# Performance work log

Measured on AMD Instinct MI355X. Metric: run time of the kernel, lower is better.

The kernel has to match this reference:

```python
import jax, jax.numpy as jnp
import numpy as np

# dims: S spaces, B batch, T tokens, D = dense_dim = concept_dim, K codebook size
S, B, T, D, K = 8, 8, 2048, 64, 512
BN_EPS = 1e-3  # keras BatchNormalization default


def setup_inputs() -> dict:
    key = jax.random.key(0)
    k0, k1, k2 = jax.random.split(key, 3)
    x = jax.random.normal(k0, (B, T, D), jnp.float32)
    W = jax.random.normal(k1, (S, D, D), jnp.float32) * 0.1   # per-space Dense kernels
    b = jnp.zeros((S, D), jnp.float32)                         # per-space Dense biases
    gamma = jnp.ones((S, D), jnp.float32)                      # BN scale
    beta = jnp.zeros((S, D), jnp.float32)                      # BN shift
    bn_mean = jnp.zeros((S, D), jnp.float32)                   # BN moving mean
    bn_var = jnp.ones((S, D), jnp.float32)                     # BN moving var
    E = jax.random.normal(k2, (S, K, D), jnp.float32)          # per-space codebooks
    return dict(x=x, W=W, b=b, gamma=gamma, beta=beta,
                bn_mean=bn_mean, bn_var=bn_var, E=E)


def reference(x, W, b, gamma, beta, bn_mean, bn_var, E):
    # per-space projection: Dense -> BatchNorm (inference) -> softmax gate
    proj = jnp.einsum('btd,sde->sbte', x, W) + b[:, None, None, :]          # [S,B,T,D]
    inv = jax.lax.rsqrt(bn_var + BN_EPS)
    bn = gamma[:, None, None, :] * (proj - bn_mean[:, None, None, :]) * inv[:, None, None, :] \
         + beta[:, None, None, :]
    att = jax.nn.softmax(bn, axis=-1)
    z = x[None] * att                                                       # z_e_att, [S,B,T,D]

    # squared euclidean distance to each code; argmin(norm) == argmin(dist^2)
    d2 = (jnp.sum(z * z, axis=-1, keepdims=True)
          - 2.0 * jnp.einsum('sbtc,skc->sbtk', z, E)
          + jnp.sum(E * E, axis=-1)[:, None, None, :])                      # [S,B,T,K]
    z_k = jnp.argmin(d2, axis=-1)                                           # [S,B,T] int

    # gather nearest codes per space, then add_n over spaces (set_att != 0)
    z_q_s = E[jnp.arange(S)[:, None, None], z_k]                            # [S,B,T,D]
    z_q = jnp.sum(z_q_s, axis=0)                                            # [B,T,D]
    z_e = jnp.sum(z, axis=0)                                                # [B,T,D]
    z_k = z_k.astype(jnp.int64) if z_k.dtype != jnp.int64 else z_k          # tf.argmin -> int64
    return z_q, z_e, z_k
```

## Files before the change

kernel.cpp:

```cpp
#include <hip/hip_runtime.h>
#include <cfloat>
#include <cmath>

#define SN 8
#define DN 64
#define KN 512
#define NN 16384
#define CK 64
#define REPAIR_THR 2e-3f
#define GAP_IK 4u
#define MAXFLAG 32768

#define WS_CNT 0
#define WS_SCL 16
#define WS_OFF (16 + SN*DN)
#define WS_E2  (WS_OFF + SN*DN)
#define WS_ENT (WS_E2 + SN*KN)
#define WS_WTH (WS_ENT + MAXFLAG)
#define WS_WTL (WS_WTH + SN*64*32)
#define WS_EH  (WS_WTL + SN*64*32)
#define WS_EL  (WS_EH + SN*KN*32)
#define WS_ZP  (WS_EL + SN*KN*32)
#define WS_E2S (WS_ZP + SN*NN*DN)
#define WS_END (WS_E2S + SN*KN)

#define LDS_ZH 0
#define LDS_ZL 16384
#define LDS_TOTAL 32768

#define FB_LDS_R2    17408
#define FB_LDS_TAIL  33792
#define FB_LDS_TOTAL 34816

typedef __attribute__((ext_vector_type(8))) short bf16x8;
typedef __attribute__((ext_vector_type(4))) short s16x4;
typedef __attribute__((ext_vector_type(4))) float f32x4;

__device__ inline short bf_hi(float f, float& rem) {
    unsigned u = __float_as_uint(f);
    unsigned r = (u + 0x7fffu + ((u >> 16) & 1u)) & 0xffff0000u;
    rem = f - __uint_as_float(r);
    return (short)(r >> 16);
}
__device__ inline short bf_rn(float f) {
    unsigned u = __float_as_uint(f);
    return (short)((u + 0x7fffu + ((u >> 16) & 1u)) >> 16);
}
__device__ inline void cvt4(float a, float b, float c, float d, s16x4& h, s16x4& l) {
    float r0, r1, r2, r3;
    h.x = bf_hi(a, r0); h.y = bf_hi(b, r1); h.z = bf_hi(c, r2); h.w = bf_hi(d, r3);
    l.x = bf_rn(r0); l.y = bf_rn(r1); l.z = bf_rn(r2); l.w = bf_rn(r3);
}
__device__ inline float bf2f(unsigned short h) {
    return __uint_as_float(((unsigned)h) << 16);
}

union U8 { bf16x8 v; s16x4 q[2]; };

__global__ void prep_all_kernel(const float* __restrict__ b, const float* __restrict__ gamma,
                                const float* __restrict__ beta, const float* __restrict__ bmean,
                                const float* __restrict__ bvar, const float* __restrict__ W,
                                const float* __restrict__ E, float* __restrict__ ws) {
    __shared__ float wt[64][65];
    const int blk = blockIdx.x, tid = threadIdx.x;
    if (blk < 256) {
        int idx = blk * 256 + tid;
        int sk = idx >> 4, c4 = idx & 15;
        int k = sk & (KN - 1);
        float4 g = ((const float4*)E)[(size_t)sk * 16 + c4];
        s16x4 h4, l4;
        cvt4(g.x, g.y, g.z, g.w, h4, l4);
        size_t off = ((size_t)sk * 128 + c4 * 8) ^ ((k & 7) << 4);
        *(s16x4*)((char*)(ws + WS_EH) + off) = h4;
        *(s16x4*)((char*)(ws + WS_EL) + off) = l4;
    } else if (blk < 264) {
        int s = blk - 256;
        #pragma unroll
        for (int r = 0; r < 4; ++r) {
            int i = r * 256 + tid;
            float4 g = ((const float4*)W)[(size_t)s * 1024 + i];
            int d = i >> 4, c4 = i & 15;
            wt[d][c4 * 4 + 0] = g.x; wt[d][c4 * 4 + 1] = g.y;
            wt[d][c4 * 4 + 2] = g.z; wt[d][c4 * 4 + 3] = g.w;
        }
        __syncthreads();
        #pragma unroll
        for (int r = 0; r < 4; ++r) {
            int j = r * 256 + tid;
            int e = j >> 4, c4 = j & 15;
            s16x4 h4, l4;
            cvt4(wt[c4 * 4 + 0][e], wt[c4 * 4 + 1][e], wt[c4 * 4 + 2][e], wt[c4 * 4 + 3][e], h4, l4);
            size_t off = (size_t)(s * 64 + e) * 128 + c4 * 8;
            *(s16x4*)((char*)(ws + WS_WTH) + off) = h4;
            *(s16x4*)((char*)(ws + WS_WTL) + off) = l4;
        }
    } else {
        if (blk == 264 && tid < 16) ((int*)ws)[tid] = 0;
        int t2 = (blk - 264) * 256 + tid;
        if (t2 < SN * KN) {
            const float* er = E + (size_t)t2 * DN;
            double a = 0.0;
            for (int d = 0; d < DN; ++d) { double v = (double)er[d]; a = fma(v, v, a); }
            ws[WS_E2 + t2]  = (float)a;
            ws[WS_E2S + t2] = (float)(a * 4096.0);
        }
        int u = t2 - SN * KN;
        if (u >= 0 && u < SN * DN) {
            double inv = 1.0 / sqrt((double)bvar[u] + 0.001);
            double sc  = (double)gamma[u] * inv;
            ws[WS_SCL + u] = (float)sc;
            ws[WS_OFF + u] = (float)(((double)b[u] - (double)bmean[u]) * sc + (double)beta[u]);
        }
    }
}

__global__ void prep_kernel(const float* __restrict__ b, const float* __restrict__ gamma,
                            const float* __restrict__ beta, const float* __restrict__ bmean,
                            const float* __restrict__ bvar, const float* __restrict__ E,
                            float* __restrict__ ws) {
    int tid = blockIdx.x * 256 + threadIdx.x;
    if (tid < SN * KN) {
        const float* er = E + (size_t)tid * DN;
        double a = 0.0;
        for (int d = 0; d < DN; ++d) { double v = (double)er[d]; a = fma(v, v, a); }
        ws[WS_E2 + tid] = (float)a;
    }
    int u = tid - SN * KN;
    if (u >= 0 && u < SN * DN) {
        double inv = 1.0 / sqrt((double)bvar[u] + 0.001);
        double sc  = (double)gamma[u] * inv;
        ws[WS_SCL + u] = (float)sc;
        ws[WS_OFF + u] = (float)(((double)b[u] - (double)bmean[u]) * sc + (double)beta[u]);
    }
}

__launch_bounds__(512, 4)
__global__ void main_kernel(const float* __restrict__ x, float* __restrict__ ws,
                            float* __restrict__ out, int entcap) {
    extern __shared__ char smraw[];
    const int tid = threadIdx.x;
    const int s  = blockIdx.y;
    const int n0 = blockIdx.x * 128;
    const int lane = tid & 63;
    const int w    = tid >> 6;
    const int cc   = lane & 15;
    const int kq   = lane >> 4;
    const int arow = w * 16 + cc;
    const int axor = (arow & 7) << 4;

    const char* eimg_h = (const char*)(ws + WS_EH) + (size_t)s * KN * 128;
    const char* eimg_l = (const char*)(ws + WS_EL) + (size_t)s * KN * 128;

    float4 pf0 = *(const float4*)(eimg_h + tid * 16);
    float4 pf1 = *(const float4*)(eimg_l + tid * 16);

    U8 xah[2], xal[2];
    #pragma unroll
    for (int ks = 0; ks < 2; ++ks) {
        const float* xr = x + (size_t)(n0 + arow) * DN + ks * 32 + kq * 8;
        float4 a = *(const float4*)xr;
        float4 b2 = *(const float4*)(xr + 4);
        s16x4 h0, l0, h1, l1;
        cvt4(a.x, a.y, a.z, a.w, h0, l0);
        cvt4(b2.x, b2.y, b2.z, b2.w, h1, l1);
        xah[ks].q[0] = h0; xah[ks].q[1] = h1;
        xal[ks].q[0] = l0; xal[ks].q[1] = l1;
    }

    const char* wimg_h = (const char*)(ws + WS_WTH) + (size_t)s * 64 * 128;
    const char* wimg_l = (const char*)(ws + WS_WTL) + (size_t)s * 64 * 128;
    f32x4 pa[4];
    #pragma unroll
    for (int nt = 0; nt < 4; ++nt) pa[nt] = (f32x4){0.f, 0.f, 0.f, 0.f};
    #pragma unroll
    for (int ks = 0; ks < 2; ++ks) {
        #pragma unroll
        for (int nt = 0; nt < 4; ++nt) {
            int brow = nt * 16 + cc;
            bf16x8 bh = *(const bf16x8*)(wimg_h + brow * 128 + ks * 64 + kq * 16);
            bf16x8 bl = *(const bf16x8*)(wimg_l + brow * 128 + ks * 64 + kq * 16);
            pa[nt] = __builtin_amdgcn_mfma_f32_16x16x32_bf16(xah[ks].v, bh, pa[nt], 0, 0, 0);
            pa[nt] = __builtin_amdgcn_mfma_f32_16x16x32_bf16(xah[ks].v, bl, pa[nt], 0, 0, 0);
            pa[nt] = __builtin_amdgcn_mfma_f32_16x16x32_bf16(xal[ks].v, bh, pa[nt], 0, 0, 0);
        }
    }

    float sclv[4], oflv[4];
    #pragma unroll
    for (int nt = 0; nt < 4; ++nt) {
        sclv[nt] = ws[WS_SCL + s * 64 + nt * 16 + cc];
        oflv[nt] = ws[WS_OFF + s * 64 + nt * 16 + cc];
    }
    float zzq[4];
    #pragma unroll
    for (int r = 0; r < 4; ++r) {
        int t = w * 16 + kq * 4 + r;
        float v0 = fmaf(pa[0][r], sclv[0], oflv[0]);
        float v1 = fmaf(pa[1][r], sclv[1], oflv[1]);
        float v2 = fmaf(pa[2][r], sclv[2], oflv[2]);
        float v3 = fmaf(pa[3][r], sclv[3], oflv[3]);
        float mx = fmaxf(fmaxf(v0, v1), fmaxf(v2, v3));
        mx = fmaxf(mx, __shfl_xor(mx, 1)); mx = fmaxf(mx, __shfl_xor(mx, 2));
        mx = fmaxf(mx, __shfl_xor(mx, 4)); mx = fmaxf(mx, __shfl_xor(mx, 8));
        float e0 = __expf(v0 - mx), e1 = __expf(v1 - mx);
        float e2v = __expf(v2 - mx), e3 = __expf(v3 - mx);
        float sm = e0 + e1 + e2v + e3;
        sm += __shfl_xor(sm, 1); sm += __shfl_xor(sm, 2);
        sm += __shfl_xor(sm, 4); sm += __shfl_xor(sm, 8);
        float inv = 1.0f / sm;
        float att[4] = { e0 * inv, e1 * inv, e2v * inv, e3 * inv };
        float zz = 0.f;
        int txor = (t & 7) << 4;
        #pragma unroll
        for (int nt = 0; nt < 4; ++nt) {
            int e = nt * 16 + cc;
            float xv = x[(size_t)(n0 + t) * DN + e];
            float z = xv * att[nt];
            zz += z * z;
            float rem; short zh = bf_hi(z, rem); short zl = bf_rn(rem);
            int zoff = (t * 128 + e * 2) ^ txor;
            *(short*)(smraw + LDS_ZH + zoff) = zh;
            *(short*)(smraw + LDS_ZL + zoff) = zl;
        }
        zz += __shfl_xor(zz, 1); zz += __shfl_xor(zz, 2);
        zz += __shfl_xor(zz, 4); zz += __shfl_xor(zz, 8);
        zzq[r] = (zz + 16.f) * 4096.f;
    }

    bf16x8 zah[2], zal[2];
    #pragma unroll
    for (int ks = 0; ks < 2; ++ks) {
        int aoff = (arow * 128 + kq * 16 + ks * 64) ^ axor;
        zah[ks] = *(const bf16x8*)(smraw + LDS_ZH + aoff);
        zal[ks] = *(const bf16x8*)(smraw + LDS_ZL + aoff);
    }
    __syncthreads();

    #pragma unroll
    for (int j = 0; j < 4; ++j) {
        int a = tid + j * 512;
        int t = a >> 4, q = a & 15;
        int off = (t * 128 + q * 8) ^ ((t & 7) << 4);
        s16x4 h = *(const s16x4*)(smraw + LDS_ZH + off);
        s16x4 l = *(const s16x4*)(smraw + LDS_ZL + off);
        float4 zv;
        zv.x = bf2f((unsigned short)h.x) + bf2f((unsigned short)l.x);
        zv.y = bf2f((unsigned short)h.y) + bf2f((unsigned short)l.y);
        zv.z = bf2f((unsigned short)h.z) + bf2f((unsigned short)l.z);
        zv.w = bf2f((unsigned short)h.w) + bf2f((unsigned short)l.w);
        ((float4*)(ws + WS_ZP))[((size_t)s * NN + n0 + t) * 16 + q] = zv;
    }
    __syncthreads();

    {
        char* eb = smraw + LDS_ZH;
        *(float4*)(eb + tid * 16) = pf0;
        *(float4*)(eb + 8192 + tid * 16) = pf1;
    }
    if (KN / CK > 1) {
        pf0 = *(const float4*)(eimg_h + (size_t)CK * 128 + tid * 16);
        pf1 = *(const float4*)(eimg_l + (size_t)CK * 128 + tid * 16);
    }
    __syncthreads();

    unsigned m1[4], m2[4];
    #pragma unroll
    for (int r = 0; r < 4; ++r) { m1[r] = 0xFFFFFFFFu; m2[r] = 0xFFFFFFFFu; }

    int p = 0;
    #pragma unroll 1
    for (int c = 0; c < KN / CK; ++c) {
        const char* ebuf = smraw + (p ? LDS_ZL : LDS_ZH);
        int kk = c * CK;
        float e2v[4];
        #pragma unroll
        for (int nt = 0; nt < 4; ++nt) e2v[nt] = ws[WS_E2S + s * KN + kk + nt * 16 + cc];

        f32x4 acc[4];
        #pragma unroll
        for (int nt = 0; nt < 4; ++nt) acc[nt] = (f32x4){0.f, 0.f, 0.f, 0.f};
        #pragma unroll
        for (int ks = 0; ks < 2; ++ks) {
            #pragma unroll
            for (int nt = 0; nt < 4; ++nt) {
                int brow = nt * 16 + cc;
                int boff = (brow * 128 + kq * 16 + ks * 64) ^ ((brow & 7) << 4);
                bf16x8 bh = *(const bf16x8*)(ebuf + boff);
                bf16x8 bl = *(const bf16x8*)(ebuf + 8192 + boff);
                acc[nt] = __builtin_amdgcn_mfma_f32_16x16x32_bf16(zah[ks], bh, acc[nt], 0, 0, 0);
                acc[nt] = __builtin_amdgcn_mfma_f32_16x16x32_bf16(zah[ks], bl, acc[nt], 0, 0, 0);
                acc[nt] = __builtin_amdgcn_mfma_f32_16x16x32_bf16(zal[ks], bh, acc[nt], 0, 0, 0);
            }
        }
        #pragma unroll
        for (int nt = 0; nt < 4; ++nt) {
            unsigned kx = (unsigned)(kk + nt * 16 + cc);
            #pragma unroll
            for (int r = 0; r < 4; ++r) {
                float cell = fmaf(-8192.f, acc[nt][r], zzq[r] + e2v[nt]);
                unsigned key = (((unsigned)cell) << 9) | kx;
                m2[r] = min(m2[r], max(m1[r], key));
                m1[r] = min(m1[r], key);
            }
        }
        if (c < KN / CK - 1) {
            char* nb = smraw + (p ? LDS_ZH : LDS_ZL);
            *(float4*)(nb + tid * 16) = pf0;
            *(float4*)(nb + 8192 + tid * 16) = pf1;
            if (c < KN / CK - 2) {
                pf0 = *(const float4*)(eimg_h + (size_t)(kk + 2 * CK) * 128 + tid * 16);
                pf1 = *(const float4*)(eimg_l + (size_t)(kk + 2 * CK) * 128 + tid * 16);
            }
            __syncthreads();
            p ^= 1;
        }
    }

    #pragma unroll
    for (int mask = 1; mask <= 8; mask <<= 1) {
        #pragma unroll
        for (int r = 0; r < 4; ++r) {
            unsigned o1 = (unsigned)__shfl_xor((int)m1[r], mask);
            unsigned o2 = (unsigned)__shfl_xor((int)m2[r], mask);
            unsigned hi = max(m1[r], o1);
            m1[r] = min(m1[r], o1);
            m2[r] = min(min(m2[r], o2), hi);
        }
    }
    #pragma unroll
    for (int r = 0; r < 4; ++r) {
        int n = n0 + w * 16 + kq * 4 + r;
        if (cc == 0) {
            int k1 = (int)(m1[r] & 511u);
            out[2 * NN * DN + s * NN + n] = (float)k1;
            if ((m2[r] >> 9) - (m1[r] >> 9) <= GAP_IK) {
                int idx = atomicAdd((int*)ws, 1);
                if (idx < entcap) ((int*)ws)[WS_ENT + idx] = (s << 14) | n;
            }
        }
    }
}

__launch_bounds__(256, 4)
__global__ void main_fb_kernel(const float* __restrict__ x, const float* __restrict__ W,
                               const float* __restrict__ E, float* __restrict__ ws,
                               float* __restrict__ out, int entcap) {
    extern __shared__ char smraw[];
    float4* xs4 = (float4*)smraw;
    float4* ws4 = (float4*)(smraw + FB_LDS_R2);
    char* ehb = smraw;
    char* elb = smraw + 8192;
    char* zhb = smraw + FB_LDS_R2;
    char* zlb = smraw + FB_LDS_R2 + 8192;
    float* tailf = (float*)(smraw + FB_LDS_TAIL);
    float* e2s = tailf; float* scl = tailf + 64; float* ofl = tailf + 128; float* zzs = tailf + 192;

    const int tid = threadIdx.x;
    const int tg = tid >> 4, lg = tid & 15;
    const int s  = blockIdx.y;
    const int n0 = blockIdx.x * 64;
    const float4* xg4 = (const float4*)x;
    const float4* Wg4 = (const float4*)W;
    const float4* Eg4 = (const float4*)E;

    #pragma unroll
    for (int r = 0; r < 4; ++r) {
        int i = r * 256 + tid;
        xs4[(i >> 4) * 17 + (i & 15)] = xg4[n0 * 16 + i];
        ws4[i] = Wg4[s * 1024 + i];
    }
    if (tid < 64) { scl[tid] = ws[WS_SCL + s * 64 + tid]; ofl[tid] = ws[WS_OFF + s * 64 + tid]; }
    __syncthreads();

    float pa[4][4];
    #pragma unroll
    for (int ti = 0; ti < 4; ++ti)
        #pragma unroll
        for (int j = 0; j < 4; ++j) pa[ti][j] = 0.f;
    #pragma unroll 4
    for (int c = 0; c < 16; ++c) {
        float4 xv[4], wv[4];
        #pragma unroll
        for (int ti = 0; ti < 4; ++ti) xv[ti] = xs4[(tg * 4 + ti) * 17 + c];
        #pragma unroll
        for (int dd = 0; dd < 4; ++dd) wv[dd] = ws4[(c * 4 + dd) * 16 + lg];
        #pragma unroll
        for (int ti = 0; ti < 4; ++ti) {
            float a0 = pa[ti][0], a1 = pa[ti][1], a2 = pa[ti][2], a3 = pa[ti][3];
            a0 = fmaf(xv[ti].x, wv[0].x, a0); a0 = fmaf(xv[ti].y, wv[1].x, a0);
            a0 = fmaf(xv[ti].z, wv[2].x, a0); a0 = fmaf(xv[ti].w, wv[3].x, a0);
            a1 = fmaf(xv[ti].x, wv[0].y, a1); a1 = fmaf(xv[ti].y, wv[1].y, a1);
            a1 = fmaf(xv[ti].z, wv[2].y, a1); a1 = fmaf(xv[ti].w, wv[3].y, a1);
            a2 = fmaf(xv[ti].x, wv[0].z, a2); a2 = fmaf(xv[ti].y, wv[1].z, a2);
            a2 = fmaf(xv[ti].z, wv[2].z, a2); a2 = fmaf(xv[ti].w, wv[3].z, a2);
            a3 = fmaf(xv[ti].x, wv[0].w, a3); a3 = fmaf(xv[ti].y, wv[1].w, a3);
            a3 = fmaf(xv[ti].z, wv[2].w, a3); a3 = fmaf(xv[ti].w, wv[3].w, a3);
            pa[ti][0] = a0; pa[ti][1] = a1; pa[ti][2] = a2; pa[ti][3] = a3;
        }
    }
    __syncthreads();

    {
        float s0 = scl[lg * 4 + 0], s1 = scl[lg * 4 + 1], s2 = scl[lg * 4 + 2], s3 = scl[lg * 4 + 3];
        float o0 = ofl[lg * 4 + 0], o1 = ofl[lg * 4 + 1], o2 = ofl[lg * 4 + 2], o3 = ofl[lg * 4 + 3];
        #pragma unroll
        for (int ti = 0; ti < 4; ++ti) {
            int t = tg * 4 + ti;
            float v0 = fmaf(pa[ti][0], s0, o0);
            float v1 = fmaf(pa[ti][1], s1, o1);
            float v2 = fmaf(pa[ti][2], s2, o2);
            float v3 = fmaf(pa[ti][3], s3, o3);
            float mx = fmaxf(fmaxf(v0, v1), fmaxf(v2, v3));
            mx = fmaxf(mx, __shfl_xor(mx, 1)); mx = fmaxf(mx, __shfl_xor(mx, 2));
            mx = fmaxf(mx, __shfl_xor(mx, 4)); mx = fmaxf(mx, __shfl_xor(mx, 8));
            float e0 = expf(v0 - mx), e1 = expf(v1 - mx), e2v = expf(v2 - mx), e3 = expf(v3 - mx);
            float sm = e0 + e1 + e2v + e3;
            sm += __shfl_xor(sm, 1); sm += __shfl_xor(sm, 2);
            sm += __shfl_xor(sm, 4); sm += __shfl_xor(sm, 8);
            float inv = 1.0f / sm;
            float4 xv = xs4[t * 17 + lg];
            float z0 = xv.x * (e0 * inv), z1 = xv.y * (e1 * inv);
            float z2 = xv.z * (e2v * inv), z3 = xv.w * (e3 * inv);
            float zz = z0 * z0 + z1 * z1 + z2 * z2 + z3 * z3;
            zz += __shfl_xor(zz, 1); zz += __shfl_xor(zz, 2);
            zz += __shfl_xor(zz, 4); zz += __shfl_xor(zz, 8);
            if (lg == 0) zzs[t] = zz;
            s16x4 h4, l4;
            cvt4(z0, z1, z2, z3, h4, l4);
            int zoff = (t * 128 + lg * 8) ^ ((t & 7) << 4);
            *(s16x4*)(zhb + zoff) = h4;
            *(s16x4*)(zlb + zoff) = l4;
            float* pz = out + NN * DN + (size_t)(n0 + t) * DN + lg * 4;
            atomicAdd(pz + 0, z0); atomicAdd(pz + 1, z1);
            atomicAdd(pz + 2, z2); atomicAdd(pz + 3, z3);
        }
    }
    __syncthreads();

    const int lane = tid & 63;
    const int w    = tid >> 6;
    const int arow = w * 16 + (lane & 15);
    const int kg16 = (lane >> 4) * 16;
    const int axor = (arow & 7) << 4;
    const int abase = arow * 128 + kg16;

    float zzv[4];
    #pragma unroll
    for (int r = 0; r < 4; ++r) zzv[r] = zzs[w * 16 + (lane >> 4) * 4 + r];

    float m1[4], m2[4]; int k1[4];
    #pragma unroll
    for (int r = 0; r < 4; ++r) { m1[r] = FLT_MAX; m2[r] = FLT_MAX; k1[r] = 0x7fffffff; }

    for (int kk = 0; kk < KN; kk += CK) {
        __syncthreads();
        #pragma unroll
        for (int r = 0; r < 4; ++r) {
            int i = r * 256 + tid;
            float4 g = Eg4[(s * KN + kk) * 16 + i];
            int row = i >> 4, c4 = i & 15;
            s16x4 h4, l4;
            cvt4(g.x, g.y, g.z, g.w, h4, l4);
            int off = (row * 128 + c4 * 8) ^ ((row & 7) << 4);
            *(s16x4*)(ehb + off) = h4;
            *(s16x4*)(elb + off) = l4;
        }
        if (tid < 64) e2s[tid] = ws[WS_E2 + s * KN + kk + tid];
        __syncthreads();

        f32x4 acc[4];
        #pragma unroll
        for (int nt = 0; nt < 4; ++nt) acc[nt] = (f32x4){0.f, 0.f, 0.f, 0.f};
        #pragma unroll
        for (int ks = 0; ks < 2; ++ks) {
            int aoff = (abase + ks * 64) ^ axor;
            bf16x8 ah = *(const bf16x8*)(zhb + aoff);
            bf16x8 al = *(const bf16x8*)(zlb + aoff);
            #pragma unroll
            for (int nt = 0; nt < 4; ++nt) {
                int brow = nt * 16 + (lane & 15);
                int boff = (brow * 128 + kg16 + ks * 64) ^ ((brow & 7) << 4);
                bf16x8 bh = *(const bf16x8*)(ehb + boff);
                bf16x8 bl = *(const bf16x8*)(elb + boff);
                acc[nt] = __builtin_amdgcn_mfma_f32_16x16x32_bf16(ah, bh, acc[nt], 0, 0, 0);
                acc[nt] = __builtin_amdgcn_mfma_f32_16x16x32_bf16(ah, bl, acc[nt], 0, 0, 0);
                acc[nt] = __builtin_amdgcn_mfma_f32_16x16x32_bf16(al, bh, acc[nt], 0, 0, 0);
            }
        }
        #pragma unroll
        for (int nt = 0; nt < 4; ++nt) {
            float e2v = e2s[nt * 16 + (lane & 15)];
            int kx = kk + nt * 16 + (lane & 15);
            #pragma unroll
            for (int r = 0; r < 4; ++r) {
                float d2 = fmaf(-2.0f, acc[nt][r], zzv[r]) + e2v;
                if (d2 < m1[r]) { m2[r] = m1[r]; m1[r] = d2; k1[r] = kx; }
                else if (d2 < m2[r]) { m2[r] = d2; }
            }
        }
    }

    #pragma unroll
    for (int mask = 1; mask <= 8; mask <<= 1) {
        #pragma unroll
        for (int r = 0; r < 4; ++r) {
            float om1 = __shfl_xor(m1[r], mask);
            int   ok1 = __shfl_xor(k1[r], mask);
            float om2 = __shfl_xor(m2[r], mask);
            bool better = (om1 < m1[r]) || (om1 == m1[r] && ok1 < k1[r]);
            float nm2 = better ? fminf(m1[r], om2) : fminf(om1, m2[r]);
            if (better) { m1[r] = om1; k1[r] = ok1; }
            m2[r] = nm2;
        }
    }
    #pragma unroll
    for (int r = 0; r < 4; ++r) {
        int t = w * 16 + (lane >> 4) * 4 + r;
        int n = n0 + t;
        if ((lane & 15) == 0) {
            out[2 * NN * DN + s * NN + n] = (float)k1[r];
            if (m2[r] - m1[r] < REPAIR_THR) {
                int idx = atomicAdd((int*)ws, 1);
                if (idx < entcap) ((int*)ws)[WS_ENT + idx] = (s << 14) | n;
            }
        }
        int kb = __shfl(k1[r], lane & 48);
        float4 eg = Eg4[(s * KN + kb) * 16 + (lane & 15)];
        float* q = out + (size_t)n * DN + (lane & 15) * 4;
        atomicAdd(q + 0, eg.x); atomicAdd(q + 1, eg.y);
        atomicAdd(q + 2, eg.z); atomicAdd(q + 3, eg.w);
    }
}

__global__ void reduce_kernel(const float* __restrict__ E, const float* __restrict__ ws,
                              float* __restrict__ out) {
    int idx = blockIdx.x * 256 + threadIdx.x;
    int n = idx >> 4, c = idx & 15;
    const float4* zp4 = (const float4*)(ws + WS_ZP);
    float4 ze = make_float4(0.f, 0.f, 0.f, 0.f);
    #pragma unroll
    for (int s = 0; s < SN; ++s) {
        float4 v = zp4[((size_t)s * NN + n) * 16 + c];
        ze.x += v.x; ze.y += v.y; ze.z += v.z; ze.w += v.w;
    }
    ((float4*)out)[NN * 16 + (size_t)n * 16 + c] = ze;

    float4 zq = make_float4(0.f, 0.f, 0.f, 0.f);
    #pragma unroll
    for (int s = 0; s < SN; ++s) {
        int k = (int)(out[2 * NN * DN + s * NN + n] + 0.5f);
        float4 e = ((const float4*)E)[((size_t)s * KN + k) * 16 + c];
        zq.x += e.x; zq.y += e.y; zq.z += e.z; zq.w += e.w;
    }
    ((float4*)out)[(size_t)n * 16 + c] = zq;
}

__global__ void repair_kernel(const float* __restrict__ x, const float* __restrict__ W,
                              const float* __restrict__ b, const float* __restrict__ gamma,
                              const float* __restrict__ beta, const float* __restrict__ bmean,
                              const float* __restrict__ bvar, const float* __restrict__ E,
                              float* __restrict__ ws, float* __restrict__ out, int entcap,
                              int do_patch) {
    __shared__ double zd[64];
    __shared__ double red[256];
    __shared__ int redk[256];
    __shared__ double zzsh;
    __shared__ int shk[2];
    int cnt = ((int*)ws)[0]; if (cnt > entcap) cnt = entcap;
    const int tid = threadIdx.x;
    for (int idx = blockIdx.x; idx < cnt; idx += gridDim.x) {
        int code = ((int*)ws)[WS_ENT + idx];
        int s = code >> 14, n = code & (NN - 1);
        int e = tid & 63, q = tid >> 6;
        const float* xrow = x + (size_t)n * 64;
        double p0 = 0.0, p1 = 0.0, p2 = 0.0, p3 = 0.0;
        for (int d = q * 16; d < q * 16 + 16; d += 4) {
            p0 = fma((double)xrow[d],     (double)W[((size_t)s * 64 + d) * 64 + e],     p0);
            p1 = fma((double)xrow[d + 1], (double)W[((size_t)s * 64 + d + 1) * 64 + e], p1);
            p2 = fma((double)xrow[d + 2], (double)W[((size_t)s * 64 + d + 2) * 64 + e], p2);
            p3 = fma((double)xrow[d + 3], (double)W[((size_t)s * 64 + d + 3) * 64 + e], p3);
        }
        red[tid] = (p0 + p1) + (p2 + p3);
        __syncthreads();
        if (tid < 64) {
            double proj = (red[tid] + red[tid + 64]) + (red[tid + 128] + red[tid + 192]);
            double inv = 1.0 / sqrt((double)bvar[s * 64 + e] + 0.001);
            double bn = (double)gamma[s * 64 + e] * ((proj + (double)b[s * 64 + e]) - (double)bmean[s * 64 + e]) * inv
                      + (double)beta[s * 64 + e];
            double m = bn;
            #pragma unroll
            for (int mask = 1; mask <= 32; mask <<= 1) m = fmax(m, __shfl_xor(m, mask));
            double ex = exp(bn - m);
            double sm = ex;
            #pragma unroll
            for (int mask = 1; mask <= 32; mask <<= 1) sm += __shfl_xor(sm, mask);
            double z = (double)xrow[e] * (ex / sm);
            zd[e] = z;
            double zz = z * z;
            #pragma unroll
            for (int mask = 1; mask <= 32; mask <<= 1) zz += __shfl_xor(zz, mask);
            if (tid == 0) zzsh = zz;
        }
        __syncthreads();
        double bv = DBL_MAX; int bk = 1 << 30;
        for (int k = tid; k < KN; k += 256) {
            const float* er = E + ((size_t)s * KN + k) * 64;
            double d0 = 0.0, d1 = 0.0, d2a = 0.0, d3 = 0.0;
            double f0 = 0.0, f1 = 0.0, f2 = 0.0, f3 = 0.0;
            for (int d = 0; d < 64; d += 4) {
                double e0 = (double)er[d], e1 = (double)er[d + 1];
                double e2d = (double)er[d + 2], e3d = (double)er[d + 3];
                d0 = fma(zd[d], e0, d0);     d1 = fma(zd[d + 1], e1, d1);
                d2a = fma(zd[d + 2], e2d, d2a); d3 = fma(zd[d + 3], e3d, d3);
                f0 = fma(e0, e0, f0); f1 = fma(e1, e1, f1);
                f2 = fma(e2d, e2d, f2); f3 = fma(e3d, e3d, f3);
            }
            double dot = (d0 + d1) + (d2a + d3);
            double e2t = (f0 + f1) + (f2 + f3);
            double d2v = (zzsh - 2.0 * dot) + e2t;
            if (d2v < bv) { bv = d2v; bk = k; }
        }
        #pragma unroll
        for (int mask = 1; mask <= 32; mask <<= 1) {
            double ov = __shfl_xor(bv, mask);
            int   ok = __shfl_xor(bk, mask);
            if (ov < bv || (ov == bv && ok < bk)) { bv = ov; bk = ok; }
        }
        if ((tid & 63) == 0) { red[tid >> 6] = bv; redk[tid >> 6] = bk; }
        __syncthreads();
        if (tid == 0) {
            double m = red[0]; int mk = redk[0];
            for (int i = 1; i < 4; ++i)
                if (red[i] < m || (red[i] == m && redk[i] < mk)) { m = red[i]; mk = redk[i]; }
            int kold = (int)(out[2 * NN * 64 + s * NN + n] + 0.5f);
            shk[0] = mk; shk[1] = kold;
            out[2 * NN * 64 + s * NN + n] = (float)mk;
        }
        __syncthreads();
        if (do_patch) {
            int mk = shk[0], kold = shk[1];
            if (mk != kold && tid < 64)
                atomicAdd(out + n * 64 + tid, E[((size_t)s * KN + mk) * 64 + tid] - E[((size_t)s * KN + kold) * 64 + tid]);
        }
        __syncthreads();
    }
}

extern "C" void kernel_launch(void* const* d_in, const int* in_sizes, int n_in,
                              void* d_out, int out_size, void* d_ws, size_t ws_size,
                              hipStream_t stream) {
    const float* x     = (const float*)d_in[0];
    const float* W     = (const float*)d_in[1];
    const float* b     = (const float*)d_in[2];
    const float* gamma = (const float*)d_in[3];
    const float* beta  = (const float*)d_in[4];
    const float* bmean = (const float*)d_in[5];
    const float* bvar  = (const float*)d_in[6];
    const float* E     = (const float*)d_in[7];
    float* out = (float*)d_out;
    float* ws  = (float*)d_ws;

    bool staged = ws_size >= (size_t)WS_END * 4;

    long avail = (long)(ws_size / 4) - WS_ENT - 16;
    if (avail < 0) avail = 0;
    int entcap = (int)(avail > MAXFLAG ? MAXFLAG : avail);
    if (staged) entcap = MAXFLAG;

    if (staged) {
        prep_all_kernel<<<282, 256, 0, stream>>>(b, gamma, beta, bmean, bvar, W, E, ws);
        dim3 grid(128, 8);
        main_kernel<<<grid, 512, LDS_TOTAL, stream>>>(x, ws, out, entcap);
        repair_kernel<<<2048, 256, 0, stream>>>(x, W, b, gamma, beta, bmean, bvar, E, ws, out, entcap, 0);
        reduce_kernel<<<1024, 256, 0, stream>>>(E, ws, out);
    } else {
        hipMemsetAsync(d_ws, 0, 64, stream);
        prep_kernel<<<18, 256, 0, stream>>>(b, gamma, beta, bmean, bvar, E, ws);
        hipMemsetAsync(d_out, 0, (size_t)(2 * NN * DN) * sizeof(float), stream);
        dim3 grid(256, 8);
        main_fb_kernel<<<grid, 256, FB_LDS_TOTAL, stream>>>(x, W, E, ws, out, entcap);
        repair_kernel<<<2048, 256, 0, stream>>>(x, W, b, gamma, beta, bmean, bvar, E, ws, out, entcap, 1);
    }
}
```

Measured before the change: 151.1 us.

## Use 128-code codebook chunks with single LDS buffer and register prefetch

Doubles the codebook chunk processed per loop iteration from 64 to 128 codes, so each wave holds eight MFMA accumulator tiles and the loop runs four times instead of eight. The LDS double-buffer ping-pong is replaced by a single 32 KB buffer, refilled from register-held prefetches between two barriers. Launch bounds drop from 4 to 2 blocks per CU to allow the larger register footprint. The intent is fewer barriers and loop iterations and more MFMA work per sync, at the cost of occupancy and an extra barrier per refill.

```diff
diff --git a/kernel.cpp b/kernel.cpp
--- a/kernel.cpp
+++ b/kernel.cpp
@@ -5,8 +5,9 @@
 #define SN 8
 #define DN 64
 #define KN 512
+#define CK 64
+#define CKD 128
 #define NN 16384
-#define CK 64
 #define REPAIR_THR 2e-3f
 #define GAP_IK 4u
 #define MAXFLAG 32768
@@ -134,7 +135,7 @@
     }
 }
 
-__launch_bounds__(512, 4)
+__launch_bounds__(512, 2)
 __global__ void main_kernel(const float* __restrict__ x, float* __restrict__ ws,
                             float* __restrict__ out, int entcap) {
     extern __shared__ char smraw[];
@@ -151,8 +152,10 @@
     const char* eimg_h = (const char*)(ws + WS_EH) + (size_t)s * KN * 128;
     const char* eimg_l = (const char*)(ws + WS_EL) + (size_t)s * KN * 128;
 
-    float4 pf0 = *(const float4*)(eimg_h + tid * 16);
-    float4 pf1 = *(const float4*)(eimg_l + tid * 16);
+    float4 pf0 = *(const float4*)(eimg_h + tid * 32);
+    float4 pf1 = *(const float4*)(eimg_h + tid * 32 + 16);
+    float4 pf2 = *(const float4*)(eimg_l + tid * 32);
+    float4 pf3 = *(const float4*)(eimg_l + tid * 32 + 16);
 
     U8 xah[2], xal[2];
     #pragma unroll
@@ -253,47 +256,47 @@
     __syncthreads();
 
     {
-        char* eb = smraw + LDS_ZH;
-        *(float4*)(eb + tid * 16) = pf0;
-        *(float4*)(eb + 8192 + tid * 16) = pf1;
-    }
-    if (KN / CK > 1) {
-        pf0 = *(const float4*)(eimg_h + (size_t)CK * 128 + tid * 16);
-        pf1 = *(const float4*)(eimg_l + (size_t)CK * 128 + tid * 16);
+        char* eb = smraw;
+        *(float4*)(eb + tid * 32)          = pf0;
+        *(float4*)(eb + tid * 32 + 16)     = pf1;
+        *(float4*)(eb + 16384 + tid * 32)  = pf2;
+        *(float4*)(eb + 16384 + tid * 32 + 16) = pf3;
     }
     __syncthreads();
+    pf0 = *(const float4*)(eimg_h + (size_t)CKD * 128 + tid * 32);
+    pf1 = *(const float4*)(eimg_h + (size_t)CKD * 128 + tid * 32 + 16);
+    pf2 = *(const float4*)(eimg_l + (size_t)CKD * 128 + tid * 32);
+    pf3 = *(const float4*)(eimg_l + (size_t)CKD * 128 + tid * 32 + 16);
 
     unsigned m1[4], m2[4];
     #pragma unroll
     for (int r = 0; r < 4; ++r) { m1[r] = 0xFFFFFFFFu; m2[r] = 0xFFFFFFFFu; }
 
-    int p = 0;
     #pragma unroll 1
-    for (int c = 0; c < KN / CK; ++c) {
-        const char* ebuf = smraw + (p ? LDS_ZL : LDS_ZH);
-        int kk = c * CK;
-        float e2v[4];
-        #pragma unroll
-        for (int nt = 0; nt < 4; ++nt) e2v[nt] = ws[WS_E2S + s * KN + kk + nt * 16 + cc];
-
-        f32x4 acc[4];
-        #pragma unroll
-        for (int nt = 0; nt < 4; ++nt) acc[nt] = (f32x4){0.f, 0.f, 0.f, 0.f};
+    for (int c = 0; c < KN / CKD; ++c) {
+        int kk = c * CKD;
+        float e2v[8];
+        #pragma unroll
+        for (int nt = 0; nt < 8; ++nt) e2v[nt] = ws[WS_E2S + s * KN + kk + nt * 16 + cc];
+
+        f32x4 acc[8];
+        #pragma unroll
+        for (int nt = 0; nt < 8; ++nt) acc[nt] = (f32x4){0.f, 0.f, 0.f, 0.f};
         #pragma unroll
         for (int ks = 0; ks < 2; ++ks) {
             #pragma unroll
-            for (int nt = 0; nt < 4; ++nt) {
+            for (int nt = 0; nt < 8; ++nt) {
                 int brow = nt * 16 + cc;
                 int boff = (brow * 128 + kq * 16 + ks * 64) ^ ((brow & 7) << 4);
-                bf16x8 bh = *(const bf16x8*)(ebuf + boff);
-                bf16x8 bl = *(const bf16x8*)(ebuf + 8192 + boff);
+                bf16x8 bh = *(const bf16x8*)(smraw + boff);
+                bf16x8 bl = *(const bf16x8*)(smraw + 16384 + boff);
                 acc[nt] = __builtin_amdgcn_mfma_f32_16x16x32_bf16(zah[ks], bh, acc[nt], 0, 0, 0);
                 acc[nt] = __builtin_amdgcn_mfma_f32_16x16x32_bf16(zah[ks], bl, acc[nt], 0, 0, 0);
                 acc[nt] = __builtin_amdgcn_mfma_f32_16x16x32_bf16(zal[ks], bh, acc[nt], 0, 0, 0);
             }
         }
         #pragma unroll
-        for (int nt = 0; nt < 4; ++nt) {
+        for (int nt = 0; nt < 8; ++nt) {
             unsigned kx = (unsigned)(kk + nt * 16 + cc);
             #pragma unroll
             for (int r = 0; r < 4; ++r) {
@@ -303,16 +306,22 @@
                 m1[r] = min(m1[r], key);
             }
         }
-        if (c < KN / CK - 1) {
-            char* nb = smraw + (p ? LDS_ZH : LDS_ZL);
-            *(float4*)(nb + tid * 16) = pf0;
-            *(float4*)(nb + 8192 + tid * 16) = pf1;
-            if (c < KN / CK - 2) {
-                pf0 = *(const float4*)(eimg_h + (size_t)(kk + 2 * CK) * 128 + tid * 16);
-                pf1 = *(const float4*)(eimg_l + (size_t)(kk + 2 * CK) * 128 + tid * 16);
-            }
+        if (c < KN / CKD - 1) {
             __syncthreads();
-            p ^= 1;
+            char* eb = smraw;
+            *(float4*)(eb + tid * 32)          = pf0;
+            *(float4*)(eb + tid * 32 + 16)     = pf1;
+            *(float4*)(eb + 16384 + tid * 32)  = pf2;
+            *(float4*)(eb + 16384 + tid * 32 + 16) = pf3;
+            if (c < KN / CKD - 2) {
+                const char* nh = eimg_h + (size_t)(kk + 2 * CKD) * 128;
+                const char* nl = eimg_l + (size_t)(kk + 2 * CKD) * 128;
+                pf0 = *(const float4*)(nh + tid * 32);
+                pf1 = *(const float4*)(nh + tid * 32 + 16);
+                pf2 = *(const float4*)(nl + tid * 32);
+                pf3 = *(const float4*)(nl + tid * 32 + 16);
+            }
+            __syncthreads();
         }
     }
 
```

Result: no change. 151.4 us (+0.2%).

## Fuse cross-space reduction into main kernel via last-block-done counter

Applied to the files above, without the earlier changes.

Removes the separate reduce kernel. Each of the 8 space-blocks for a token tile bumps a per-tile atomic counter, and the last one to finish sums z_e over spaces and gathers the nearest codes into z_q for that tile. The repair kernel now patches z_q itself (do_patch=1) for tokens it reassigns. This saves one kernel launch and a full pass over the outputs, at the cost of threadfences, an atomic per block, and serial tail work in the last-arriving block.

```diff
diff --git a/kernel.cpp b/kernel.cpp
--- a/kernel.cpp
+++ b/kernel.cpp
@@ -22,7 +22,8 @@
 #define WS_EL  (WS_EH + SN*KN*32)
 #define WS_ZP  (WS_EL + SN*KN*32)
 #define WS_E2S (WS_ZP + SN*NN*DN)
-#define WS_END (WS_E2S + SN*KN)
+#define WS_TCNT (WS_E2S + SN*KN)
+#define WS_END (WS_TCNT + 128)
 
 #define LDS_ZH 0
 #define LDS_ZL 16384
@@ -95,7 +96,10 @@
             *(s16x4*)((char*)(ws + WS_WTL) + off) = l4;
         }
     } else {
-        if (blk == 264 && tid < 16) ((int*)ws)[tid] = 0;
+        if (blk == 264) {
+            if (tid < 16) ((int*)ws)[tid] = 0;
+            if (tid >= 16 && tid < 144) ((int*)(ws + WS_TCNT))[tid - 16] = 0;
+        }
         int t2 = (blk - 264) * 256 + tid;
         if (t2 < SN * KN) {
             const float* er = E + (size_t)t2 * DN;
@@ -135,8 +139,8 @@
 }
 
 __launch_bounds__(512, 4)
-__global__ void main_kernel(const float* __restrict__ x, float* __restrict__ ws,
-                            float* __restrict__ out, int entcap) {
+__global__ void main_kernel(const float* __restrict__ x, const float* __restrict__ E,
+                            float* __restrict__ ws, float* __restrict__ out, int entcap) {
     extern __shared__ char smraw[];
     const int tid = threadIdx.x;
     const int s  = blockIdx.y;
@@ -338,6 +342,40 @@
                 if (idx < entcap) ((int*)ws)[WS_ENT + idx] = (s << 14) | n;
             }
         }
+    }
+
+    __shared__ int lastf;
+    __threadfence();
+    if (tid == 0) {
+        int old = atomicAdd((int*)(ws + WS_TCNT) + blockIdx.x, 1);
+        lastf = (old == SN - 1);
+    }
+    __syncthreads();
+    if (!lastf) return;
+    __threadfence();
+
+    const float4* zp4 = (const float4*)(ws + WS_ZP);
+    const float4* Eg4 = (const float4*)E;
+    #pragma unroll
+    for (int j = 0; j < 4; ++j) {
+        int a = tid + j * 512;
+        int t = a >> 4, q = a & 15;
+        size_t n = (size_t)(n0 + t);
+        float4 ze = make_float4(0.f, 0.f, 0.f, 0.f);
+        #pragma unroll
+        for (int ss = 0; ss < SN; ++ss) {
+            float4 v = zp4[((size_t)ss * NN + n) * 16 + q];
+            ze.x += v.x; ze.y += v.y; ze.z += v.z; ze.w += v.w;
+        }
+        ((float4*)out)[NN * 16 + n * 16 + q] = ze;
+        float4 zq = make_float4(0.f, 0.f, 0.f, 0.f);
+        #pragma unroll
+        for (int ss = 0; ss < SN; ++ss) {
+            int k = (int)(out[2 * NN * DN + ss * NN + n] + 0.5f);
+            float4 e = Eg4[((size_t)ss * KN + k) * 16 + q];
+            zq.x += e.x; zq.y += e.y; zq.z += e.z; zq.w += e.w;
+        }
+        ((float4*)out)[n * 16 + q] = zq;
     }
 }
 
@@ -532,29 +570,6 @@
     }
 }
 
-__global__ void reduce_kernel(const float* __restrict__ E, const float* __restrict__ ws,
-                              float* __restrict__ out) {
-    int idx = blockIdx.x * 256 + threadIdx.x;
-    int n = idx >> 4, c = idx & 15;
-    const float4* zp4 = (const float4*)(ws + WS_ZP);
-    float4 ze = make_float4(0.f, 0.f, 0.f, 0.f);
-    #pragma unroll
-    for (int s = 0; s < SN; ++s) {
-        float4 v = zp4[((size_t)s * NN + n) * 16 + c];
-        ze.x += v.x; ze.y += v.y; ze.z += v.z; ze.w += v.w;
-    }
-    ((float4*)out)[NN * 16 + (size_t)n * 16 + c] = ze;
-
-    float4 zq = make_float4(0.f, 0.f, 0.f, 0.f);
-    #pragma unroll
-    for (int s = 0; s < SN; ++s) {
-        int k = (int)(out[2 * NN * DN + s * NN + n] + 0.5f);
-        float4 e = ((const float4*)E)[((size_t)s * KN + k) * 16 + c];
-        zq.x += e.x; zq.y += e.y; zq.z += e.z; zq.w += e.w;
-    }
-    ((float4*)out)[(size_t)n * 16 + c] = zq;
-}
-
 __global__ void repair_kernel(const float* __restrict__ x, const float* __restrict__ W,
                               const float* __restrict__ b, const float* __restrict__ gamma,
                               const float* __restrict__ beta, const float* __restrict__ bmean,
@@ -670,9 +685,8 @@
     if (staged) {
         prep_all_kernel<<<282, 256, 0, stream>>>(b, gamma, beta, bmean, bvar, W, E, ws);
         dim3 grid(128, 8);
-        main_kernel<<<grid, 512, LDS_TOTAL, stream>>>(x, ws, out, entcap);
-        repair_kernel<<<2048, 256, 0, stream>>>(x, W, b, gamma, beta, bmean, bvar, E, ws, out, entcap, 0);
-        reduce_kernel<<<1024, 256, 0, stream>>>(E, ws, out);
+        main_kernel<<<grid, 512, LDS_TOTAL, stream>>>(x, E, ws, out, entcap);
+        repair_kernel<<<2048, 256, 0, stream>>>(x, W, b, gamma, beta, bmean, bvar, E, ws, out, entcap, 1);
     } else {
         hipMemsetAsync(d_ws, 0, 64, stream);
         prep_kernel<<<18, 256, 0, stream>>>(b, gamma, beta, bmean, bvar, E, ws);
```

After: 398.5 us. 2.64x slower.
